# Kernel optimization log

Hardware: AMD Instinct MI355X
Metric: run time of the kernel (lower is better)

Reference implementation:

```python
import jax, jax.numpy as jnp
import numpy as np

N = 20000      # nodes
E = 320000     # edges (avg degree 16)
IN = 128
HID = 64
CLS = 32
H0, H1, H2 = 4, 4, 6
SLOPE = 0.2


def _lin(key, fan_in, fan_out):
    kw, kb = jax.random.split(key)
    s = 1.0 / np.sqrt(fan_in)
    W = jax.random.uniform(kw, (fan_in, fan_out), minval=-s, maxval=s, dtype=jnp.float32)
    b = jax.random.uniform(kb, (fan_out,), minval=-s, maxval=s, dtype=jnp.float32)
    return W, b


def setup_inputs() -> dict:
    key = jax.random.key(0)
    ks = jax.random.split(key, 16)
    x = jax.random.normal(ks[0], (N, IN), dtype=jnp.float32)
    src = jax.random.randint(ks[1], (E,), 0, N)
    dst = jax.random.randint(ks[2], (E,), 0, N)
    W0s, b0s = _lin(ks[3], IN, H0 * HID)
    W0d, b0d = _lin(ks[4], IN, H0 * HID)
    a0 = jax.random.normal(ks[5], (H0, HID), dtype=jnp.float32) * 0.05
    d1 = H0 * HID  # 256, flattened hidden width
    W1s, b1s = _lin(ks[6], d1, H1 * HID)
    W1d, b1d = _lin(ks[7], d1, H1 * HID)
    a1 = jax.random.normal(ks[8], (H1, HID), dtype=jnp.float32) * 0.05
    W2s, b2s = _lin(ks[9], d1, H2 * CLS)
    W2d, b2d = _lin(ks[10], d1, H2 * CLS)
    a2 = jax.random.normal(ks[11], (H2, CLS), dtype=jnp.float32) * 0.05
    Wr2, br2 = _lin(ks[12], d1, H2 * CLS)  # residual projection (256 != 192)
    return dict(x=x, src=src, dst=dst,
                W0s=W0s, b0s=b0s, W0d=W0d, b0d=b0d, a0=a0,
                W1s=W1s, b1s=b1s, W1d=W1d, b1d=b1d, a1=a1,
                W2s=W2s, b2s=b2s, W2d=W2d, b2d=b2d, a2=a2,
                Wr2=Wr2, br2=br2)


def _gatv2_layer(x, src, dst, Ws, bs, Wd, bd, attn, heads, dim, res, act):
    n = x.shape[0]
    feat_src = (x @ Ws + bs).reshape(n, heads, dim)
    feat_dst = (x @ Wd + bd).reshape(n, heads, dim)
    # GATv2 edge scores: a^T LeakyReLU(W_l h_u + W_r h_v)
    e = jax.nn.leaky_relu(feat_src[src] + feat_dst[dst], SLOPE)  # [E,H,D]
    logits = jnp.einsum('ehd,hd->eh', e, attn)                    # [E,H]
    # numerically-stable edge softmax over incoming edges per destination
    m = jax.ops.segment_max(logits, dst, num_segments=n)
    m = jnp.where(jnp.isfinite(m), m, 0.0)
    ex = jnp.exp(logits - m[dst])
    denom = jax.ops.segment_sum(ex, dst, num_segments=n)
    alpha = ex / denom[dst]                                        # [E,H]
    out = jax.ops.segment_sum(feat_src[src] * alpha[:, :, None], dst, num_segments=n)
    if res == 'id':
        out = out + x.reshape(n, heads, dim)
    elif res is not None:
        Wr, br = res
        out = out + (x @ Wr + br).reshape(n, heads, dim)
    if act:
        out = jax.nn.elu(out)
    return out  # [n, heads, dim]


def reference(x, src, dst,
              W0s, b0s, W0d, b0d, a0,
              W1s, b1s, W1d, b1d, a1,
              W2s, b2s, W2d, b2d, a2,
              Wr2, br2):
    h = _gatv2_layer(x, src, dst, W0s, b0s, W0d, b0d, a0, H0, HID, None, True)
    h = h.reshape(N, H0 * HID)
    h = _gatv2_layer(h, src, dst, W1s, b1s, W1d, b1d, a1, H1, HID, 'id', True)
    h = h.reshape(N, H1 * HID)
    out = _gatv2_layer(h, src, dst, W2s, b2s, W2d, b2d, a2, H2, CLS, (Wr2, br2), False)
    return out.mean(axis=1)  # [N, num_classes]
```

## Files before the change

kernel.cpp:

```cpp
#include <hip/hip_runtime.h>
#include <hip/hip_bf16.h>
#include <float.h>
#include <math.h>

#define NN 20000
#define EE 320000
#define IN_DIM 128
#define DEG_CAP 64

typedef __attribute__((ext_vector_type(4))) float f32x4;
typedef _Float16 f16;
typedef __attribute__((ext_vector_type(2))) _Float16 f16x2;
typedef __attribute__((ext_vector_type(4))) _Float16 f16x4;
typedef __attribute__((ext_vector_type(8))) _Float16 f16x8;

typedef const unsigned int __attribute__((address_space(1)))* gas_u32p;
typedef unsigned int __attribute__((address_space(3)))* las_u32p;

__device__ __forceinline__ void prep_elem(const float* __restrict__ Wa, const float* __restrict__ ba, int na,
                                          const float* __restrict__ Wb, const float* __restrict__ bb, int nb,
                                          const float* __restrict__ Wc, const float* __restrict__ bc, int nc,
                                          int K, f16* __restrict__ Wt, float* __restrict__ bias_cat, int idx) {
    int n = idx / K;
    int k = idx - n * K;
    const float* W; const float* b; int nl; int ncols;
    if (n < na) { W = Wa; b = ba; nl = n; ncols = na; }
    else if (n < na + nb) { W = Wb; b = bb; nl = n - na; ncols = nb; }
    else { W = Wc; b = bc; nl = n - na - nb; ncols = nc; }
    Wt[(size_t)n * K + k] = (f16)W[(size_t)k * ncols + nl];
    if (k == 0) bias_cat[n] = b[nl];
}

#define SEG0 (512 * 128)
#define SEG1 (512 * 256)
#define SEG2 (576 * 256)
#define SEG3 (NN * IN_DIM / 4)
__global__ void prep_all(const float* __restrict__ W0s, const float* __restrict__ b0s,
                         const float* __restrict__ W0d, const float* __restrict__ b0d,
                         const float* __restrict__ W1s, const float* __restrict__ b1s,
                         const float* __restrict__ W1d, const float* __restrict__ b1d,
                         const float* __restrict__ W2s, const float* __restrict__ b2s,
                         const float* __restrict__ W2d, const float* __restrict__ b2d,
                         const float* __restrict__ Wr2, const float* __restrict__ br2,
                         const float* __restrict__ x,
                         f16* __restrict__ Wt0, float* __restrict__ bias0,
                         f16* __restrict__ Wt1, float* __restrict__ bias1,
                         f16* __restrict__ Wt2, float* __restrict__ bias2,
                         f16* __restrict__ A) {
    int idx = blockIdx.x * 256 + threadIdx.x;
    if (idx < SEG0) {
        prep_elem(W0s, b0s, 256, W0d, b0d, 256, nullptr, nullptr, 0, 128, Wt0, bias0, idx);
    } else if ((idx -= SEG0) < SEG1) {
        prep_elem(W1s, b1s, 256, W1d, b1d, 256, nullptr, nullptr, 0, 256, Wt1, bias1, idx);
    } else if ((idx -= SEG1) < SEG2) {
        prep_elem(W2s, b2s, 192, W2d, b2d, 192, Wr2, br2, 192, 256, Wt2, bias2, idx);
    } else if ((idx -= SEG2) < SEG3) {
        float4 v = ((const float4*)x)[idx];
        f16x4 o = {(f16)v.x, (f16)v.y, (f16)v.z, (f16)v.w};
        ((f16x4*)A)[idx] = o;
    }
}

__global__ __launch_bounds__(256) void gemm_mfma_f16(
        const f16* __restrict__ A, const f16* __restrict__ Wt,
        const float* __restrict__ bias,
        f16* __restrict__ F0, f16* __restrict__ F1, float* __restrict__ F2,
        int b1, int b2, int M, int K, int S, int gx, int gy,
        int GB, const int* __restrict__ esrc, const int* __restrict__ edst,
        unsigned int* __restrict__ cursor, int* __restrict__ csr_dst, int E) {
    __shared__ f16 Bs[64 * 256];

    const int bid = blockIdx.x;
    if (bid >= GB) {
        int e = (bid - GB) * 256 + threadIdx.x;
        if (e < E) {
            int d = edst[e];
            unsigned pos = atomicAdd(&cursor[d], 1u);
            if (pos < DEG_CAP) csr_dst[(unsigned)d * DEG_CAP + pos] = esrc[e];
        }
        return;
    }

    const int p = bid & 7;
    const int q = bid >> 3;
    const int bn_i = q % gx;
    const int bm_i = (q / gx) * 8 + p;
    if (bm_i >= gy) return;
    const int bm = bm_i * 128;
    const int bn = bn_i * 64;

    const int tid = threadIdx.x;
    const int wave = tid >> 6;
    const int lane = tid & 63;
    const int m16 = lane & 15;
    const int quad = lane >> 4;

    {
        const f16* gs = Wt + (size_t)(bn + 16 * wave + (lane & 15)) * K + (lane >> 4) * 8;
        #pragma unroll
        for (int j = 0; j * 32 < K; ++j) {
            __builtin_amdgcn_global_load_lds(
                (gas_u32p)(const void*)(gs + j * 32),
                (las_u32p)(void*)(&Bs[((j * 4 + wave) * 64) * 8]),
                16, 0, 0);
        }
    }
    __syncthreads();

    const int rb0 = bm + wave * 32;
    f32x4 acc[2][4];
    #pragma unroll
    for (int mt = 0; mt < 2; ++mt)
        #pragma unroll
        for (int nt = 0; nt < 4; ++nt) acc[mt][nt] = (f32x4){0.f, 0.f, 0.f, 0.f};

    int ar[2];
    #pragma unroll
    for (int mt = 0; mt < 2; ++mt) {
        int row = rb0 + mt * 16 + m16;
        ar[mt] = row < M ? row : M - 1;
    }

    #pragma unroll 4
    for (int k0 = 0; k0 < K; k0 += 32) {
        f16x8 bs[4];
        #pragma unroll
        for (int nt = 0; nt < 4; ++nt)
            bs[nt] = *(const f16x8*)&Bs[(((k0 >> 5) * 4 + nt) * 64 + lane) * 8];
        f16x8 ah[2];
        #pragma unroll
        for (int mt = 0; mt < 2; ++mt)
            ah[mt] = *(const f16x8*)(A + (size_t)ar[mt] * K + k0 + quad * 8);
        #pragma unroll
        for (int nt = 0; nt < 4; ++nt)
            #pragma unroll
            for (int mt = 0; mt < 2; ++mt)
                acc[mt][nt] = __builtin_amdgcn_mfma_f32_16x16x32_f16(ah[mt], bs[nt], acc[mt][nt], 0, 0, 0);
    }

    __syncthreads();
    f16* Cs = Bs;

    if (bn < b2) {
        f16* __restrict__ Fb;
        int cs, cb;
        if (bn >= b1) { Fb = F1; cb = bn - b1; cs = b2 - b1; }
        else          { Fb = F0; cb = bn;      cs = b1; }
        f16* cw = Cs + wave * (32 * 66);
        #pragma unroll
        for (int nt = 0; nt < 4; ++nt) {
            float bv = bias[bn + nt * 16 + m16];
            #pragma unroll
            for (int mt = 0; mt < 2; ++mt)
                #pragma unroll
                for (int r = 0; r < 4; ++r) {
                    int row = mt * 16 + quad * 4 + r;
                    cw[row * 66 + nt * 16 + m16] = (f16)(acc[mt][nt][r] + bv);
                }
        }
        int lrow = lane >> 1;
        int lcol = (lane & 1) * 32;
        int grow = rb0 + lrow;
        if (grow < M) {
            #pragma unroll
            for (int j = 0; j < 4; ++j) {
                f16x8 v = *(f16x8*)&cw[lrow * 66 + lcol + j * 8];
                *(f16x8*)&Fb[(size_t)grow * cs + cb + lcol + j * 8] = v;
            }
        }
    } else {
        int cs = S - b2;
        #pragma unroll
        for (int nt = 0; nt < 4; ++nt) {
            int col = bn - b2 + nt * 16 + m16;
            float bv = bias[bn + nt * 16 + m16];
            #pragma unroll
            for (int mt = 0; mt < 2; ++mt)
                #pragma unroll
                for (int r = 0; r < 4; ++r) {
                    int row = rb0 + mt * 16 + quad * 4 + r;
                    if (row < M) F2[(size_t)row * cs + col] = acc[mt][nt][r] + bv;
                }
        }
    }
}

#define AGG_STEP(U0, CNT)                                                     \
    _Pragma("unroll")                                                         \
    for (int uu = 0; uu < (CNT); ++uu) {                                      \
        const int u = (U0) + uu;                                              \
        const f16x8 cur = buf[u];                                             \
        unsigned su = (unsigned)cidx[u]; su = su < NN ? su : 0u;              \
        buf[u] = *(const f16x8*)&fsb[su * (unsigned)HD + off];                \
        cidx[u] = csr_l[nib64 + min(b + 16 + u, dgm1)];                       \
        float pp = 0.f;                                                       \
        _Pragma("unroll")                                                     \
        for (int i = 0; i < 4; ++i) {                                         \
            f16x2 cp = (f16x2){cur[2 * i], cur[2 * i + 1]};                   \
            f16x2 xp = cp + fdp[i];                                           \
            unsigned xu = __builtin_bit_cast(unsigned, xp) & 0x7FFF7FFFu;     \
            f16x2 xa = __builtin_bit_cast(f16x2, xu);                         \
            pp = __builtin_amdgcn_fdot2(xp, a6p[i], pp, false);               \
            pp = __builtin_amdgcn_fdot2(xa, a4p[i], pp, false);               \
        }                                                                     \
        _Pragma("unroll")                                                     \
        for (int o = 1; o < GSZ; o <<= 1) pp += __shfl_xor(pp, o, 64);        \
        float w = (b + u < dg) ? __expf(pp) : 0.f;                            \
        lh += w;                                                              \
        _Pragma("unroll")                                                     \
        for (int d = 0; d < 8; ++d) acc[d] += w * (float)cur[d];              \
    }

template <int HD, int D, bool HAS_RES, bool DO_ELU, int OUT_MODE>
__global__ __launch_bounds__(256) void gat_node_aggregate(
        const f16* __restrict__ fsb, const f16* __restrict__ fdb,
        const float* __restrict__ attn,
        const unsigned int* __restrict__ degv,
        const int* __restrict__ csr_src,
        const float* __restrict__ resid, int RS,
        float* __restrict__ outF, f16* __restrict__ outA) {
    constexpr int LANES = HD / 8;
    constexpr int GSZ = D / 8;
    __shared__ int csr_l[512];
    __shared__ float red[(OUT_MODE == 2) ? 8 : 1][(OUT_MODE == 2) ? HD : 1];

    {
        int i = threadIdx.x;
        csr_l[i]       = csr_src[(size_t)blockIdx.x * 512 + i];
        csr_l[i + 256] = csr_src[(size_t)blockIdx.x * 512 + i + 256];
    }

    const int wave = threadIdx.x >> 6;
    const int lane = threadIdx.x & 63;
    const int half = lane >> 5;
    const int ln = lane & 31;
    const int t = blockIdx.x * 8 + wave * 2 + half;
    const bool active = (ln < LANES);
    const unsigned off = active ? 8u * ln : 0u;
    const int nib64 = (wave * 2 + half) * 64;

    f16x2 fdp[4], a6p[4], a4p[4];
    if (active) {
        f16x8 dv = *(const f16x8*)&fdb[(unsigned)t * HD + off];
        float4 aA = *(const float4*)&attn[off];
        float4 aB = *(const float4*)&attn[off + 4];
        float av[8] = {aA.x, aA.y, aA.z, aA.w, aB.x, aB.y, aB.z, aB.w};
        #pragma unroll
        for (int i = 0; i < 4; ++i) {
            fdp[i] = (f16x2){dv[2 * i], dv[2 * i + 1]};
            a6p[i] = (f16x2){(f16)(0.6f * av[2 * i]), (f16)(0.6f * av[2 * i + 1])};
            a4p[i] = (f16x2){(f16)(0.4f * av[2 * i]), (f16)(0.4f * av[2 * i + 1])};
        }
    } else {
        #pragma unroll
        for (int i = 0; i < 4; ++i) {
            fdp[i] = (f16x2){0, 0}; a6p[i] = (f16x2){0, 0}; a4p[i] = (f16x2){0, 0};
        }
    }

    const int dg = min((int)degv[t], DEG_CAP);
    const int dgm1 = max(dg - 1, 0);
    const int degO = __shfl_xor(dg, 32, 64);
    const int mdeg = max(dg, degO);

    float acc[8];
    #pragma unroll
    for (int d = 0; d < 8; ++d) acc[d] = 0.f;
    float lh = 0.f;

    __syncthreads();

    f16x8 buf[8];
    int cidx[8];
    #pragma unroll
    for (int u = 0; u < 8; ++u) {
        unsigned s0 = (unsigned)csr_l[nib64 + min(u, dgm1)];
        s0 = s0 < NN ? s0 : 0u;
        buf[u] = *(const f16x8*)&fsb[s0 * (unsigned)HD + off];
        cidx[u] = csr_l[nib64 + min(8 + u, dgm1)];
    }

    int b = 0;
    for (; b + 8 <= mdeg; b += 8) {
        AGG_STEP(0, 4)
        AGG_STEP(4, 4)
    }
    {
        const int rem = mdeg - b;
        if (rem > 0) { AGG_STEP(0, 2) }
        if (rem > 2) { AGG_STEP(2, 2) }
        if (rem > 4) { AGG_STEP(4, 2) }
        if (rem > 6) { AGG_STEP(6, 2) }
    }

    float inv = (lh > 0.f) ? 1.f / lh : 0.f;
    float vout[8];
    #pragma unroll
    for (int d = 0; d < 8; ++d) vout[d] = acc[d] * inv;
    if (HAS_RES && active) {
        float4 rA = *(const float4*)&resid[(unsigned)t * RS + off];
        float4 rB = *(const float4*)&resid[(unsigned)t * RS + off + 4];
        vout[0] += rA.x; vout[1] += rA.y; vout[2] += rA.z; vout[3] += rA.w;
        vout[4] += rB.x; vout[5] += rB.y; vout[6] += rB.z; vout[7] += rB.w;
    }
    if (DO_ELU) {
        #pragma unroll
        for (int d = 0; d < 8; ++d) vout[d] = vout[d] > 0.f ? vout[d] : expm1f(vout[d]);
    }

    if (OUT_MODE == 2) {
        const int nib = wave * 2 + half;
        if (active) {
            *(float4*)&red[nib][off] = make_float4(vout[0], vout[1], vout[2], vout[3]);
            *(float4*)&red[nib][off + 4] = make_float4(vout[4], vout[5], vout[6], vout[7]);
        }
        __syncthreads();
        int node = threadIdx.x >> 5;
        int col = threadIdx.x & 31;
        float ssum = 0.f;
        #pragma unroll
        for (int h = 0; h < 6; ++h) ssum += red[node][h * 32 + col];
        outF[(unsigned)(blockIdx.x * 8 + node) * 32 + col] = ssum * (1.f / 6.f);
    } else if (active) {
        f16x8 av;
        #pragma unroll
        for (int d = 0; d < 8; ++d) av[d] = (f16)vout[d];
        *(f16x8*)&outA[(unsigned)t * HD + off] = av;
        if (OUT_MODE == 0) {
            *(float4*)&outF[(unsigned)t * HD + off] = make_float4(vout[0], vout[1], vout[2], vout[3]);
            *(float4*)&outF[(unsigned)t * HD + off + 4] = make_float4(vout[4], vout[5], vout[6], vout[7]);
        }
    }
}

extern "C" void kernel_launch(void* const* d_in, const int* in_sizes, int n_in,
                              void* d_out, int out_size, void* d_ws, size_t ws_size,
                              hipStream_t stream) {
    const float* x   = (const float*)d_in[0];
    const int*   src = (const int*)d_in[1];
    const int*   dst = (const int*)d_in[2];
    const float* W0s = (const float*)d_in[3];
    const float* b0s = (const float*)d_in[4];
    const float* W0d = (const float*)d_in[5];
    const float* b0d = (const float*)d_in[6];
    const float* a0  = (const float*)d_in[7];
    const float* W1s = (const float*)d_in[8];
    const float* b1s = (const float*)d_in[9];
    const float* W1d = (const float*)d_in[10];
    const float* b1d = (const float*)d_in[11];
    const float* a1  = (const float*)d_in[12];
    const float* W2s = (const float*)d_in[13];
    const float* b2s = (const float*)d_in[14];
    const float* W2d = (const float*)d_in[15];
    const float* b2d = (const float*)d_in[16];
    const float* a2  = (const float*)d_in[17];
    const float* Wr2 = (const float*)d_in[18];
    const float* br2 = (const float*)d_in[19];

    f16* FsH = (f16*)d_ws;
    f16* FdH = FsH + (size_t)NN * 256;
    f16* A   = FdH + (size_t)NN * 256;
    float* O0 = (float*)(A + (size_t)NN * 256);
    f16* Wt0 = (f16*)(O0 + (size_t)NN * 256);
    f16* Wt1 = Wt0 + 512 * 128;
    f16* Wt2 = Wt1 + 512 * 256;
    float* bias0 = (float*)(Wt2 + 576 * 256);
    float* bias1 = bias0 + 512;
    float* bias2 = bias1 + 512;
    unsigned int* deg = (unsigned int*)(bias2 + 576);
    int* csr_src      = (int*)(deg + NN);

    hipMemsetAsync(deg, 0, (size_t)NN * 4, stream);
    {
        int total = SEG0 + SEG1 + SEG2 + SEG3;
        prep_all<<<(total + 255) / 256, 256, 0, stream>>>(
            W0s, b0s, W0d, b0d, W1s, b1s, W1d, b1d, W2s, b2s, W2d, b2d, Wr2, br2, x,
            Wt0, bias0, Wt1, bias1, Wt2, bias2, A);
    }

    const int gy = (NN + 127) / 128;
    const int gy8 = ((gy + 7) / 8) * 8;
    const int nagg = NN / 8;
    const int sblk = (EE + 255) / 256;

    gemm_mfma_f16<<<gy8 * 8 + sblk, 256, 0, stream>>>(A, Wt0, bias0,
                                               FsH, FdH, nullptr, 256, 512, NN, 128, 512, 8, gy,
                                               gy8 * 8, src, dst, deg, csr_src, EE);
    gat_node_aggregate<256, 64, false, true, 0><<<nagg, 256, 0, stream>>>(
        FsH, FdH, a0, deg, csr_src, nullptr, 0, O0, A);

    gemm_mfma_f16<<<gy8 * 8, 256, 0, stream>>>(A, Wt1, bias1,
                                               FsH, FdH, nullptr, 256, 512, NN, 256, 512, 8, gy,
                                               gy8 * 8, nullptr, nullptr, nullptr, nullptr, 0);
    gat_node_aggregate<256, 64, true, true, 1><<<nagg, 256, 0, stream>>>(
        FsH, FdH, a1, deg, csr_src, O0, 256, nullptr, A);

    gemm_mfma_f16<<<gy8 * 9, 256, 0, stream>>>(A, Wt2, bias2,
                                               FsH, FdH, O0, 192, 384, NN, 256, 576, 9, gy,
                                               gy8 * 9, nullptr, nullptr, nullptr, nullptr, 0);
    gat_node_aggregate<192, 32, true, false, 2><<<nagg, 256, 0, stream>>>(
        FsH, FdH, a2, deg, csr_src, O0, 192, (float*)d_out, nullptr);
}
```

Baseline: 281.9 us.

## Template GEMM on K, preload A rows into registers, drop CSR index clamps

Makes the GEMM kernel a template on K. Every A fragment for the whole K range is loaded into registers before the barrier, so the global A loads overlap with the async B-to-LDS copy, and shared memory is sized per K. In the aggregation kernel the per-edge min/bounds clamps on CSR indices are removed. To keep out-of-range reads safe, the CSR buffer is zero-filled by a larger memset and the LDS index array gets 32 padding zeros. The trade-off is higher register pressure in the GEMM, plus a much bigger memset (about 5 MB) on every call.

```diff
diff --git a/kernel.cpp b/kernel.cpp
--- a/kernel.cpp
+++ b/kernel.cpp
@@ -61,14 +61,17 @@
     }
 }
 
+template <int K>
 __global__ __launch_bounds__(256) void gemm_mfma_f16(
         const f16* __restrict__ A, const f16* __restrict__ Wt,
         const float* __restrict__ bias,
         f16* __restrict__ F0, f16* __restrict__ F1, float* __restrict__ F2,
-        int b1, int b2, int M, int K, int S, int gx, int gy,
+        int b1, int b2, int M, int S, int gx, int gy,
         int GB, const int* __restrict__ esrc, const int* __restrict__ edst,
         unsigned int* __restrict__ cursor, int* __restrict__ csr_dst, int E) {
-    __shared__ f16 Bs[64 * 256];
+    constexpr int K32 = K / 32;
+    constexpr int BSN = (64 * K > 4 * 32 * 66) ? 64 * K : 4 * 32 * 66;
+    __shared__ f16 Bs[BSN];
 
     const int bid = blockIdx.x;
     if (bid >= GB) {
@@ -96,24 +99,17 @@
     const int quad = lane >> 4;
 
     {
-        const f16* gs = Wt + (size_t)(bn + 16 * wave + (lane & 15)) * K + (lane >> 4) * 8;
-        #pragma unroll
-        for (int j = 0; j * 32 < K; ++j) {
+        const f16* gs = Wt + (size_t)(bn + 16 * wave + m16) * K + quad * 8;
+        #pragma unroll
+        for (int j = 0; j < K32; ++j) {
             __builtin_amdgcn_global_load_lds(
                 (gas_u32p)(const void*)(gs + j * 32),
                 (las_u32p)(void*)(&Bs[((j * 4 + wave) * 64) * 8]),
                 16, 0, 0);
         }
     }
-    __syncthreads();
 
     const int rb0 = bm + wave * 32;
-    f32x4 acc[2][4];
-    #pragma unroll
-    for (int mt = 0; mt < 2; ++mt)
-        #pragma unroll
-        for (int nt = 0; nt < 4; ++nt) acc[mt][nt] = (f32x4){0.f, 0.f, 0.f, 0.f};
-
     int ar[2];
     #pragma unroll
     for (int mt = 0; mt < 2; ++mt) {
@@ -121,21 +117,34 @@
         ar[mt] = row < M ? row : M - 1;
     }
 
-    #pragma unroll 4
-    for (int k0 = 0; k0 < K; k0 += 32) {
+    f16x8 ahr[2][K32];
+    #pragma unroll
+    for (int mt = 0; mt < 2; ++mt) {
+        const f16* ap = A + (size_t)ar[mt] * K + quad * 8;
+        #pragma unroll
+        for (int kc = 0; kc < K32; ++kc)
+            ahr[mt][kc] = *(const f16x8*)(ap + kc * 32);
+    }
+
+    __syncthreads();
+
+    f32x4 acc[2][4];
+    #pragma unroll
+    for (int mt = 0; mt < 2; ++mt)
+        #pragma unroll
+        for (int nt = 0; nt < 4; ++nt) acc[mt][nt] = (f32x4){0.f, 0.f, 0.f, 0.f};
+
+    #pragma unroll
+    for (int kc = 0; kc < K32; ++kc) {
         f16x8 bs[4];
         #pragma unroll
         for (int nt = 0; nt < 4; ++nt)
-            bs[nt] = *(const f16x8*)&Bs[(((k0 >> 5) * 4 + nt) * 64 + lane) * 8];
-        f16x8 ah[2];
-        #pragma unroll
-        for (int mt = 0; mt < 2; ++mt)
-            ah[mt] = *(const f16x8*)(A + (size_t)ar[mt] * K + k0 + quad * 8);
+            bs[nt] = *(const f16x8*)&Bs[((kc * 4 + nt) * 64 + lane) * 8];
         #pragma unroll
         for (int nt = 0; nt < 4; ++nt)
             #pragma unroll
             for (int mt = 0; mt < 2; ++mt)
-                acc[mt][nt] = __builtin_amdgcn_mfma_f32_16x16x32_f16(ah[mt], bs[nt], acc[mt][nt], 0, 0, 0);
+                acc[mt][nt] = __builtin_amdgcn_mfma_f32_16x16x32_f16(ahr[mt][kc], bs[nt], acc[mt][nt], 0, 0, 0);
     }
 
     __syncthreads();
@@ -190,9 +199,9 @@
     for (int uu = 0; uu < (CNT); ++uu) {                                      \
         const int u = (U0) + uu;                                              \
         const f16x8 cur = buf[u];                                             \
-        unsigned su = (unsigned)cidx[u]; su = su < NN ? su : 0u;              \
+        const unsigned su = (unsigned)cidx[u];                                \
         buf[u] = *(const f16x8*)&fsb[su * (unsigned)HD + off];                \
-        cidx[u] = csr_l[nib64 + min(b + 16 + u, dgm1)];                       \
+        cidx[u] = csr_l[nib64 + b + 16 + u];                                  \
         float pp = 0.f;                                                       \
         _Pragma("unroll")                                                     \
         for (int i = 0; i < 4; ++i) {                                         \
@@ -221,13 +230,14 @@
         float* __restrict__ outF, f16* __restrict__ outA) {
     constexpr int LANES = HD / 8;
     constexpr int GSZ = D / 8;
-    __shared__ int csr_l[512];
+    __shared__ int csr_l[544];
     __shared__ float red[(OUT_MODE == 2) ? 8 : 1][(OUT_MODE == 2) ? HD : 1];
 
     {
         int i = threadIdx.x;
         csr_l[i]       = csr_src[(size_t)blockIdx.x * 512 + i];
         csr_l[i + 256] = csr_src[(size_t)blockIdx.x * 512 + i + 256];
+        if (i < 32) csr_l[512 + i] = 0;
     }
 
     const int wave = threadIdx.x >> 6;
@@ -259,7 +269,6 @@
     }
 
     const int dg = min((int)degv[t], DEG_CAP);
-    const int dgm1 = max(dg - 1, 0);
     const int degO = __shfl_xor(dg, 32, 64);
     const int mdeg = max(dg, degO);
 
@@ -274,10 +283,9 @@
     int cidx[8];
     #pragma unroll
     for (int u = 0; u < 8; ++u) {
-        unsigned s0 = (unsigned)csr_l[nib64 + min(u, dgm1)];
-        s0 = s0 < NN ? s0 : 0u;
+        unsigned s0 = (unsigned)csr_l[nib64 + u];
         buf[u] = *(const f16x8*)&fsb[s0 * (unsigned)HD + off];
-        cidx[u] = csr_l[nib64 + min(8 + u, dgm1)];
+        cidx[u] = csr_l[nib64 + 8 + u];
     }
 
     int b = 0;
@@ -370,7 +378,7 @@
     unsigned int* deg = (unsigned int*)(bias2 + 576);
     int* csr_src      = (int*)(deg + NN);
 
-    hipMemsetAsync(deg, 0, (size_t)NN * 4, stream);
+    hipMemsetAsync(deg, 0, (size_t)NN * 4 + (size_t)NN * DEG_CAP * 4, stream);
     {
         int total = SEG0 + SEG1 + SEG2 + SEG3;
         prep_all<<<(total + 255) / 256, 256, 0, stream>>>(
@@ -383,20 +391,20 @@
     const int nagg = NN / 8;
     const int sblk = (EE + 255) / 256;
 
-    gemm_mfma_f16<<<gy8 * 8 + sblk, 256, 0, stream>>>(A, Wt0, bias0,
-                                               FsH, FdH, nullptr, 256, 512, NN, 128, 512, 8, gy,
+    gemm_mfma_f16<128><<<gy8 * 8 + sblk, 256, 0, stream>>>(A, Wt0, bias0,
+                                               FsH, FdH, nullptr, 256, 512, NN, 512, 8, gy,
                                                gy8 * 8, src, dst, deg, csr_src, EE);
     gat_node_aggregate<256, 64, false, true, 0><<<nagg, 256, 0, stream>>>(
         FsH, FdH, a0, deg, csr_src, nullptr, 0, O0, A);
 
-    gemm_mfma_f16<<<gy8 * 8, 256, 0, stream>>>(A, Wt1, bias1,
-                                               FsH, FdH, nullptr, 256, 512, NN, 256, 512, 8, gy,
+    gemm_mfma_f16<256><<<gy8 * 8, 256, 0, stream>>>(A, Wt1, bias1,
+                                               FsH, FdH, nullptr, 256, 512, NN, 512, 8, gy,
                                                gy8 * 8, nullptr, nullptr, nullptr, nullptr, 0);
     gat_node_aggregate<256, 64, true, true, 1><<<nagg, 256, 0, stream>>>(
         FsH, FdH, a1, deg, csr_src, O0, 256, nullptr, A);
 
-    gemm_mfma_f16<<<gy8 * 9, 256, 0, stream>>>(A, Wt2, bias2,
-                                               FsH, FdH, O0, 192, 384, NN, 256, 576, 9, gy,
+    gemm_mfma_f16<256><<<gy8 * 9, 256, 0, stream>>>(A, Wt2, bias2,
+                                               FsH, FdH, O0, 192, 384, NN, 576, 9, gy,
                                                gy8 * 9, nullptr, nullptr, nullptr, nullptr, 0);
     gat_node_aggregate<192, 32, true, false, 2><<<nagg, 256, 0, stream>>>(
         FsH, FdH, a2, deg, csr_src, O0, 192, (float*)d_out, nullptr);
```

Measured after the change: 269.2 us. 4.5% less time.
